# Kernel tuning notes

Hardware: AMD Instinct MI355X
Metric: run time of the kernel (lower is better)

Reference implementation:

```python
import jax, jax.numpy as jnp
import numpy as np

B = 1
T_DIM, H_DIM, W_DIM = 8, 24, 24          # video canvas (t, h, w)
TT, TH, TW = 2, 8, 8                      # tile sizes
WT, WH, WW = 6, 16, 16                    # window sizes (tokens)
HIDDEN = 1024
HEADS = 16
DH = HIDDEN // HEADS
SEQ = T_DIM * H_DIM * W_DIM               # 4608
NT, NH, NW = T_DIM // TT, H_DIM // TH, W_DIM // TW   # tile grid (4,3,3)
N_TILES = NT * NH * NW                    # 36
TILE = TT * TH * TW                       # 128


def _gather_indices():
    # STA tile mask: kv tile allowed iff |clamp(q_tile, k//2, n-1-k//2) - kv_tile| <= k//2 per axis.
    # Due to the clamp, every query tile attends to exactly the same number of kv tiles,
    # so the block-sparse pattern is a dense gather of shape [N_TILES, K].
    def axis(n, kernel_tiles):
        half = kernel_tiles // 2
        c = np.clip(np.arange(n), half, n - 1 - half)
        return c[:, None] + np.arange(-half, half + 1)[None, :]  # [n, 2*half+1]
    ts = axis(NT, WT // TT)
    hs = axis(NH, WH // TH)
    ws = axis(NW, WW // TW)
    idx = (ts[:, None, None, :, None, None] * NH
           + hs[None, :, None, None, :, None]) * NW \
          + ws[None, None, :, None, None, :]
    return idx.reshape(N_TILES, -1).astype(np.int32)  # [N_TILES, K]


def setup_inputs() -> dict:
    key = jax.random.key(0)
    k1, k2, k3, k4, k5 = jax.random.split(key, 5)
    s = 0.02
    return {
        "hidden_states": jax.random.normal(k1, (B, SEQ, HIDDEN), jnp.float32),
        "q_w": jax.random.normal(k2, (HIDDEN, HIDDEN), jnp.float32) * s,
        "k_w": jax.random.normal(k3, (HIDDEN, HIDDEN), jnp.float32) * s,
        "v_w": jax.random.normal(k4, (HIDDEN, HIDDEN), jnp.float32) * s,
        "o_w": jax.random.normal(k5, (HIDDEN, HIDDEN), jnp.float32) * s,
    }


def _tileize(x):
    # [B, S, HEADS*DH] -> [B, HEADS, N_TILES, TILE, DH] in (t,h,w) tile-major order
    x = x.reshape(B, NT, TT, NH, TH, NW, TW, HEADS, DH)
    x = x.transpose(0, 7, 1, 3, 5, 2, 4, 6, 8)
    return x.reshape(B, HEADS, N_TILES, TILE, DH)


def _untileize(x):
    # [B, HEADS, N_TILES, TILE, DH] -> [B, S, HEADS*DH]
    x = x.reshape(B, HEADS, NT, NH, NW, TT, TH, TW, DH)
    x = x.transpose(0, 2, 5, 3, 6, 4, 7, 1, 8)
    return x.reshape(B, SEQ, HEADS * DH)


def reference(hidden_states, q_w, k_w, v_w, o_w):
    q = _tileize(hidden_states @ q_w.T)
    k = _tileize(hidden_states @ k_w.T)
    v = _tileize(hidden_states @ v_w.T)
    idx = jnp.asarray(_gather_indices())          # [N_TILES, K] (static)
    kk = k[:, :, idx]                              # [B, H, N_TILES, K, TILE, DH]
    vv = v[:, :, idx]
    K = idx.shape[1]
    kk = kk.reshape(B, HEADS, N_TILES, K * TILE, DH)
    vv = vv.reshape(B, HEADS, N_TILES, K * TILE, DH)
    scale = 1.0 / np.sqrt(DH).astype(np.float32)
    scores = jnp.einsum('bhnqd,bhnkd->bhnqk', q * scale, kk)  # [B,H,nT,TILE,K*TILE]
    attn = jax.nn.softmax(scores, axis=-1)
    out = jnp.einsum('bhnqk,bhnkd->bhnqd', attn, vv)
    return _untileize(out) @ o_w.T
```

## Files before the change

kernel.cpp:

```cpp
#include <hip/hip_runtime.h>
#include <math.h>

#define HID 1024
#define NHEADS 16
#define NTILES 36
#define HEADSZ (36*128*64)
#define LOG2E 1.4426950408889634f
#define PLSTRIDE 73728

typedef unsigned short u16;
typedef unsigned int u32;
typedef __attribute__((ext_vector_type(8))) u16 ushort8v;
typedef __attribute__((ext_vector_type(8))) __bf16 bf16x8;
typedef __attribute__((ext_vector_type(16))) float f32x16;
typedef __attribute__((ext_vector_type(4))) u32 u32x4;

__device__ __forceinline__ u32 cvt_pk_bf16(float lo, float hi) {
  u32 r;
  asm("v_cvt_pk_bf16_f32 %0, %1, %2" : "=v"(r) : "v"(lo), "v"(hi));
  return r;
}
__device__ __forceinline__ void permlane32_swap(u32 &a, u32 &b) {
  asm volatile("v_permlane32_swap_b32 %0, %1" : "+v"(a), "+v"(b));
}
__device__ __forceinline__ void gld_lds16(const void* g, void* l) {
  __builtin_amdgcn_global_load_lds((const __attribute__((address_space(1))) u32*)g,
                                   (__attribute__((address_space(3))) u32*)l, 16, 0, 0);
}
__device__ __forceinline__ f32x16 mfma32(bf16x8 a, bf16x8 b, f32x16 c) {
  return __builtin_amdgcn_mfma_f32_32x32x16_bf16(a, b, c, 0, 0, 0);
}
__device__ __forceinline__ u16 bf16r(float x) {
  u32 b = __builtin_bit_cast(u32, x);
  b += 0x7fff + ((b >> 16) & 1);
  return (u16)(b >> 16);
}
__device__ __forceinline__ float bf2f(u16 v) {
  return __builtin_bit_cast(float, (u32)v << 16);
}

struct CastJob { const float* src[5]; u16* dst[5]; int n[5]; };

__global__ __launch_bounds__(256)
void cast_bf16(CastJob j) {
  const int w = blockIdx.y;
  const int n = j.n[w];
  const int i = (blockIdx.x * 256 + threadIdx.x) * 8;
  if (i >= n) return;
  const float4 v0 = *reinterpret_cast<const float4*>(j.src[w] + i);
  const float4 v1 = *reinterpret_cast<const float4*>(j.src[w] + i + 4);
  u32x4 o;
  o.x = cvt_pk_bf16(v0.x, v0.y);
  o.y = cvt_pk_bf16(v0.z, v0.w);
  o.z = cvt_pk_bf16(v1.x, v1.y);
  o.w = cvt_pk_bf16(v1.z, v1.w);
  *reinterpret_cast<u32x4*>(j.dst[w] + i) = o;
}

template<int AMODE, int CMODE, bool QKV, bool DBUF>
__global__ __launch_bounds__(256)
void gemm_mfma(const u16* __restrict__ A, const u16* __restrict__ B,
               void* __restrict__ Cv, float alpha)
{
    __shared__ __align__(16) u16 sm[DBUF ? 2 : 1][2][8192];

    const int tid = threadIdx.x;
    const int wv = tid >> 6, l = tid & 63;
    const int l31 = l & 31, hi = l >> 5;
    const int wm = wv >> 1, wn = wv & 1;
    const int by = blockIdx.y;
    const int n0 = blockIdx.x * 128;
    const float av = (QKV && n0 >= 1024) ? 1.0f : alpha;

    const int tt = by / 9, rem = by % 9, th = rem / 3, tw = rem % 3;
    const int tilebase = tt * 1152 + th * 192 + tw * 8;

    const int lrow = l >> 3;
    const int lslot = l & 7;
    const int sg = (lslot ^ lrow) * 8;
    const u16* aptr[4];
    const u16* bptr[4];
#pragma unroll
    for (int i = 0; i < 4; ++i) {
        const int row = (wv * 4 + i) * 8 + lrow;
        if (AMODE == 0) {
            const int s = tilebase + (row >> 6) * 576 + ((row >> 3) & 7) * 24 + (row & 7);
            aptr[i] = A + (size_t)s * HID + sg;
        } else {
            aptr[i] = A + (size_t)(by * 128 + row) * 64 + sg;
        }
        bptr[i] = B + (size_t)(n0 + row) * HID + sg;
    }

    auto stage = [&](int buf, int kc) {
#pragma unroll
        for (int i = 0; i < 4; ++i) {
            const u16* ga = (AMODE == 0) ? (aptr[i] + kc)
                                         : (aptr[i] + (size_t)(kc >> 6) * HEADSZ);
            gld_lds16(ga, &sm[buf][0][(wv * 4 + i) * 512]);
            gld_lds16(bptr[i] + kc, &sm[buf][1][(wv * 4 + i) * 512]);
        }
    };

    f32x16 acc[2][2];
#pragma unroll
    for (int mb = 0; mb < 2; ++mb)
#pragma unroll
        for (int nb = 0; nb < 2; ++nb)
#pragma unroll
            for (int i = 0; i < 16; ++i) acc[mb][nb][i] = 0.f;

    auto compute = [&](int buf) {
        __builtin_amdgcn_s_setprio(1);
#pragma unroll
        for (int kk = 0; kk < 4; ++kk) {
            bf16x8 af[2], bfr[2];
#pragma unroll
            for (int mb = 0; mb < 2; ++mb) {
                const int row = wm * 64 + mb * 32 + l31;
                af[mb] = *reinterpret_cast<const bf16x8*>(
                    &sm[buf][0][row * 64 + (((kk * 2 + hi) ^ (row & 7)) * 8)]);
            }
#pragma unroll
            for (int nb = 0; nb < 2; ++nb) {
                const int row = wn * 64 + nb * 32 + l31;
                bfr[nb] = *reinterpret_cast<const bf16x8*>(
                    &sm[buf][1][row * 64 + (((kk * 2 + hi) ^ (row & 7)) * 8)]);
            }
#pragma unroll
            for (int mb = 0; mb < 2; ++mb)
#pragma unroll
                for (int nb = 0; nb < 2; ++nb)
                    acc[mb][nb] = mfma32(af[mb], bfr[nb], acc[mb][nb]);
        }
        __builtin_amdgcn_s_setprio(0);
    };

    if (DBUF) {
        stage(0, 0);
        __syncthreads();
        int cur = 0;
        for (int kc = 0; kc < HID; kc += 64) {
            if (kc + 64 < HID) stage(cur ^ 1, kc + 64);
            compute(cur);
            __syncthreads();
            cur ^= 1;
        }
    } else {
        for (int kc = 0; kc < HID; kc += 64) {
            __syncthreads();
            stage(0, kc);
            __syncthreads();
            compute(0);
        }
    }

    if (CMODE == 0) {
        float* C = (float*)Cv;
#pragma unroll
        for (int mb = 0; mb < 2; ++mb)
#pragma unroll
            for (int r = 0; r < 16; ++r) {
                const int m = wm * 64 + mb * 32 + (r & 3) + 8 * (r >> 2) + 4 * hi;
                const int s = tilebase + (m >> 6) * 576 + ((m >> 3) & 7) * 24 + (m & 7);
#pragma unroll
                for (int nb = 0; nb < 2; ++nb) {
                    const int n = n0 + wn * 64 + nb * 32 + l31;
                    C[(size_t)s * HID + n] = acc[mb][nb][r] * av;
                }
            }
    } else {
        u16* C = (u16*)Cv;
#pragma unroll
        for (int mb = 0; mb < 2; ++mb)
#pragma unroll
            for (int rq = 0; rq < 4; ++rq) {
                const int mbase = wm * 64 + mb * 32 + 8 * rq + 4 * hi;
#pragma unroll
                for (int nb = 0; nb < 2; ++nb) {
                    const int n = n0 + wn * 64 + nb * 32 + l31;
                    const int head = n >> 6, dh = n & 63;
                    if (QKV && head >= 32) {
                        u32 w0 = cvt_pk_bf16(acc[mb][nb][rq * 4 + 0], acc[mb][nb][rq * 4 + 1]);
                        u32 w1 = cvt_pk_bf16(acc[mb][nb][rq * 4 + 2], acc[mb][nb][rq * 4 + 3]);
                        *reinterpret_cast<uint2*>(C + (size_t)head * HEADSZ +
                            (size_t)by * 8192 + dh * 128 + mbase) = make_uint2(w0, w1);
                    } else {
#pragma unroll
                        for (int j = 0; j < 4; ++j) {
                            const int m = mbase + j;
                            C[(size_t)head * HEADSZ + (size_t)(by * 128 + m) * 64 + dh] =
                                bf16r(acc[mb][nb][rq * 4 + j] * av);
                        }
                    }
                }
            }
    }
}

__global__ __launch_bounds__(256, 4)
void attn_mfma(const u16* __restrict__ Q, const u16* __restrict__ K,
               const u16* __restrict__ Vt, u16* __restrict__ pO0,
               u16* __restrict__ pO1, float* __restrict__ pl)
{
    __shared__ u16 sm[2][2][4096];

    const int tid = threadIdx.x;
    const int wave = tid >> 6;
    const int lane = tid & 63;
    const int l31 = lane & 31;
    const int hi  = lane >> 5;

    const int logical = (blockIdx.x & 7) * 144 + (blockIdx.x >> 3);
    const int p  = logical & 1;
    const int bt = logical >> 1;
    const int tl = bt % NTILES;
    const int hd = bt / NTILES;
    const size_t headbase = (size_t)hd * HEADSZ;

    const u16* Qg = Q + headbase + (size_t)tl * 8192;
    const u16* Kh = K + headbase;
    const u16* Vh = Vt + headbase;

    bf16x8 qf[4];
    {
        const u16* qrow = Qg + (wave * 32 + l31) * 64 + hi * 8;
#pragma unroll
        for (int ks = 0; ks < 4; ++ks)
            qf[ks] = *reinterpret_cast<const bf16x8*>(qrow + ks * 16);
    }

    const int base_t = (min(max(tl / 9, 1), 2) - 1) * 9;

    const int srow = lane >> 3;
    const int slot = lane & 7;

    auto stage = [&](int i, int bi) {
        const int kt = base_t + i;
        const u16* Kg = Kh + (size_t)kt * 8192 + p * 4096;
        const u16* Vg = Vh + (size_t)kt * 8192 + p * 64;
        u16* dk = &sm[bi][0][0];
        u16* dv = &sm[bi][1][0];
#pragma unroll
        for (int q = 0; q < 2; ++q) {
            const int seg = wave * 2 + q;
            const int key = seg * 8 + srow;
            gld_lds16(Kg + key * 64 + ((slot ^ (key & 7)) * 8), dk + seg * 512);
            const int dh = seg * 8 + srow;
            gld_lds16(Vg + dh * 128 + ((slot ^ (dh & 7)) * 8), dv + seg * 512);
        }
    };

    f32x16 accO0, accO1;
#pragma unroll
    for (int i = 0; i < 16; ++i) { accO0[i] = 0.f; accO1[i] = 0.f; }
    float lsum = 0.f;

    stage(0, 0);
    __syncthreads();

    for (int i = 0; i < 27; ++i) {
        const int cur = i & 1;
        if (i + 1 < 27) stage(i + 1, cur ^ 1);
        const u16* Ksb = &sm[cur][0][0];
        const u16* Vsb = &sm[cur][1][0];

#pragma unroll
        for (int c = 0; c < 2; ++c) {
            f32x16 s;
#pragma unroll
            for (int i2 = 0; i2 < 16; ++i2) s[i2] = 0.f;
            const int kr = c * 32 + l31;
            __builtin_amdgcn_s_setprio(1);
#pragma unroll
            for (int ks = 0; ks < 4; ++ks) {
                bf16x8 a = *reinterpret_cast<const bf16x8*>(
                    Ksb + kr * 64 + (((2 * ks + hi) ^ (kr & 7)) * 8));
                s = mfma32(a, qf[ks], s);
            }
            __builtin_amdgcn_s_setprio(0);

#pragma unroll
            for (int i2 = 0; i2 < 16; ++i2) s[i2] = __builtin_amdgcn_exp2f(s[i2]);

            float ps = 0.f;
#pragma unroll
            for (int i2 = 0; i2 < 16; ++i2) ps += s[i2];
            lsum += ps;

            bf16x8 pb[2];
            {
                u32 a0 = cvt_pk_bf16(s[0], s[1]);
                u32 a1 = cvt_pk_bf16(s[2], s[3]);
                u32 b0 = cvt_pk_bf16(s[4], s[5]);
                u32 b1 = cvt_pk_bf16(s[6], s[7]);
                permlane32_swap(a0, b0);
                permlane32_swap(a1, b1);
                u32x4 w; w.x = a0; w.y = a1; w.z = b0; w.w = b1;
                pb[0] = __builtin_bit_cast(bf16x8, w);
                u32 c0 = cvt_pk_bf16(s[8], s[9]);
                u32 c1 = cvt_pk_bf16(s[10], s[11]);
                u32 d0 = cvt_pk_bf16(s[12], s[13]);
                u32 d1 = cvt_pk_bf16(s[14], s[15]);
                permlane32_swap(c0, d0);
                permlane32_swap(c1, d1);
                u32x4 w2; w2.x = c0; w2.y = c1; w2.z = d0; w2.w = d1;
                pb[1] = __builtin_bit_cast(bf16x8, w2);
            }

            __builtin_amdgcn_s_setprio(1);
#pragma unroll
            for (int k2 = 0; k2 < 2; ++k2) {
                const int sg2 = c * 4 + k2 * 2 + hi;
                bf16x8 v0 = *reinterpret_cast<const bf16x8*>(
                    Vsb + l31 * 64 + ((sg2 ^ (l31 & 7)) * 8));
                accO0 = mfma32(v0, pb[k2], accO0);
                bf16x8 v1 = *reinterpret_cast<const bf16x8*>(
                    Vsb + (32 + l31) * 64 + ((sg2 ^ (l31 & 7)) * 8));
                accO1 = mfma32(v1, pb[k2], accO1);
            }
            __builtin_amdgcn_s_setprio(0);
        }
        __syncthreads();
    }

    lsum += __shfl_xor(lsum, 32);

    u16* Ob = (p ? pO1 : pO0) + ((size_t)bt * 128 + wave * 32 + l31) * 64;
#pragma unroll
    for (int t = 0; t < 4; ++t) {
        u32 p0 = cvt_pk_bf16(accO0[4 * t], accO0[4 * t + 1]);
        u32 p1 = cvt_pk_bf16(accO0[4 * t + 2], accO0[4 * t + 3]);
        *reinterpret_cast<uint2*>(Ob + t * 8 + 4 * hi) = make_uint2(p0, p1);
        u32 q0 = cvt_pk_bf16(accO1[4 * t], accO1[4 * t + 1]);
        u32 q1 = cvt_pk_bf16(accO1[4 * t + 2], accO1[4 * t + 3]);
        *reinterpret_cast<uint2*>(Ob + 32 + t * 8 + 4 * hi) = make_uint2(q0, q1);
    }
    if (hi == 0) pl[p * PLSTRIDE + bt * 128 + wave * 32 + l31] = lsum;
}

__global__ __launch_bounds__(256)
void merge_attn(const u16* __restrict__ pO0, const u16* __restrict__ pO1,
                const float* __restrict__ pl, u16* __restrict__ O)
{
    const int b = blockIdx.x;
    const int tid = threadIdx.x;
    const int row = tid >> 1;
    const int d0 = (tid & 1) * 32;
    const size_t rbase = ((size_t)b * 128 + row) * 64 + d0;
    const float inv = 1.f / (pl[b * 128 + row] + pl[PLSTRIDE + b * 128 + row]);
#pragma unroll
    for (int g = 0; g < 4; ++g) {
        ushort8v a = *reinterpret_cast<const ushort8v*>(pO0 + rbase + g * 8);
        ushort8v c = *reinterpret_cast<const ushort8v*>(pO1 + rbase + g * 8);
        u32 w[4];
#pragma unroll
        for (int h = 0; h < 4; ++h) {
            float f0 = (bf2f(a[2 * h])     + bf2f(c[2 * h]))     * inv;
            float f1 = (bf2f(a[2 * h + 1]) + bf2f(c[2 * h + 1])) * inv;
            w[h] = cvt_pk_bf16(f0, f1);
        }
        u32x4 st; st.x = w[0]; st.y = w[1]; st.z = w[2]; st.w = w[3];
        *reinterpret_cast<u32x4*>(O + rbase + g * 8) = st;
    }
}

extern "C" void kernel_launch(void* const* d_in, const int* in_sizes, int n_in,
                              void* d_out, int out_size, void* d_ws, size_t ws_size,
                              hipStream_t stream) {
    const float* hs = (const float*)d_in[0];
    const float* qw = (const float*)d_in[1];
    const float* kw = (const float*)d_in[2];
    const float* vw = (const float*)d_in[3];
    const float* ow = (const float*)d_in[4];
    float* out = (float*)d_out;

    const size_t TSZ = (size_t)NHEADS * HEADSZ;
    const size_t WSZ = (size_t)HID * HID;
    u16* hsb = (u16*)d_ws;
    u16* wqb = hsb + TSZ;
    u16* wkb = wqb + WSZ;
    u16* wvb = wkb + WSZ;
    u16* wob = wvb + WSZ;
    u16* qb  = wob + WSZ;
    u16* kb  = qb + TSZ;
    u16* vt  = kb + TSZ;
    u16* pO0 = hsb;
    u16* pO1 = vt + TSZ;
    float* pl = (float*)(pO1 + TSZ);
    u16* aob = (u16*)(pl + 2 * PLSTRIDE);

    CastJob cj;
    cj.src[0] = hs; cj.dst[0] = hsb; cj.n[0] = (int)TSZ;
    cj.src[1] = qw; cj.dst[1] = wqb; cj.n[1] = (int)WSZ;
    cj.src[2] = kw; cj.dst[2] = wkb; cj.n[2] = (int)WSZ;
    cj.src[3] = vw; cj.dst[3] = wvb; cj.n[3] = (int)WSZ;
    cj.src[4] = ow; cj.dst[4] = wob; cj.n[4] = (int)WSZ;
    cast_bf16<<<dim3(2304, 5), 256, 0, stream>>>(cj);

    gemm_mfma<0, 1, true, true><<<dim3(24, 36), 256, 0, stream>>>(hsb, wqb, qb, 0.125f * LOG2E);
    attn_mfma<<<NHEADS * NTILES * 2, 256, 0, stream>>>(qb, kb, vt, pO0, pO1, pl);
    merge_attn<<<NHEADS * NTILES, 256, 0, stream>>>(pO0, pO1, pl, aob);
    gemm_mfma<1, 0, false, true><<<dim3(8, 36), 256, 0, stream>>>(aob, wob, out, 1.0f);
}
```

Before: 158.7 us.

## Store V in MFMA-fragment layout and load it directly from global memory

The QKV projection epilogue now writes V transposed into a chunked layout: blocks of 8 keys, with 8 consecutive keys per head dimension stored contiguously. With that layout each lane's PV MFMA operand is one contiguous 16-byte global load. The attention kernel no longer stages V through LDS, which halves LDS traffic and footprint per stage. The cost is that V loads go to global/L2 memory inside the inner loop with no double buffering, so their latency may be exposed before the PV MFMAs.

After: 156.8 us (median of 2 runs). About the same (-1.2%).

```diff
diff --git a/kernel.cpp b/kernel.cpp
--- a/kernel.cpp
+++ b/kernel.cpp
@@ -184,7 +184,8 @@
                         u32 w0 = cvt_pk_bf16(acc[mb][nb][rq * 4 + 0], acc[mb][nb][rq * 4 + 1]);
                         u32 w1 = cvt_pk_bf16(acc[mb][nb][rq * 4 + 2], acc[mb][nb][rq * 4 + 3]);
                         *reinterpret_cast<uint2*>(C + (size_t)head * HEADSZ +
-                            (size_t)by * 8192 + dh * 128 + mbase) = make_uint2(w0, w1);
+                            (size_t)by * 8192 + (mbase >> 3) * 512 + (dh << 3) +
+                            (mbase & 7)) = make_uint2(w0, w1);
                     } else {
 #pragma unroll
                         for (int j = 0; j < 4; ++j) {
@@ -203,7 +204,7 @@
                const u16* __restrict__ Vt, u16* __restrict__ pO0,
                u16* __restrict__ pO1, float* __restrict__ pl)
 {
-    __shared__ u16 sm[2][2][4096];
+    __shared__ u16 sm[2][4096];
 
     const int tid = threadIdx.x;
     const int wave = tid >> 6;
@@ -238,16 +239,12 @@
     auto stage = [&](int i, int bi) {
         const int kt = base_t + i;
         const u16* Kg = Kh + (size_t)kt * 8192 + p * 4096;
-        const u16* Vg = Vh + (size_t)kt * 8192 + p * 64;
-        u16* dk = &sm[bi][0][0];
-        u16* dv = &sm[bi][1][0];
+        u16* dk = &sm[bi][0];
 #pragma unroll
         for (int q = 0; q < 2; ++q) {
             const int seg = wave * 2 + q;
             const int key = seg * 8 + srow;
             gld_lds16(Kg + key * 64 + ((slot ^ (key & 7)) * 8), dk + seg * 512);
-            const int dh = seg * 8 + srow;
-            gld_lds16(Vg + dh * 128 + ((slot ^ (dh & 7)) * 8), dv + seg * 512);
         }
     };
 
@@ -262,11 +259,20 @@
     for (int i = 0; i < 27; ++i) {
         const int cur = i & 1;
         if (i + 1 < 27) stage(i + 1, cur ^ 1);
-        const u16* Ksb = &sm[cur][0][0];
-        const u16* Vsb = &sm[cur][1][0];
+        const u16* Ksb = &sm[cur][0];
+        const u16* Vg = Vh + (size_t)(base_t + i) * 8192;
 
 #pragma unroll
         for (int c = 0; c < 2; ++c) {
+            bf16x8 vf[2][2];
+#pragma unroll
+            for (int k2 = 0; k2 < 2; ++k2) {
+                const int chunk = 8 * p + 4 * c + 2 * k2 + hi;
+                const u16* vb = Vg + chunk * 512 + l31 * 8;
+                vf[k2][0] = *reinterpret_cast<const bf16x8*>(vb);
+                vf[k2][1] = *reinterpret_cast<const bf16x8*>(vb + 256);
+            }
+
             f32x16 s;
 #pragma unroll
             for (int i2 = 0; i2 < 16; ++i2) s[i2] = 0.f;
@@ -311,13 +317,8 @@
             __builtin_amdgcn_s_setprio(1);
 #pragma unroll
             for (int k2 = 0; k2 < 2; ++k2) {
-                const int sg2 = c * 4 + k2 * 2 + hi;
-                bf16x8 v0 = *reinterpret_cast<const bf16x8*>(
-                    Vsb + l31 * 64 + ((sg2 ^ (l31 & 7)) * 8));
-                accO0 = mfma32(v0, pb[k2], accO0);
-                bf16x8 v1 = *reinterpret_cast<const bf16x8*>(
-                    Vsb + (32 + l31) * 64 + ((sg2 ^ (l31 & 7)) * 8));
-                accO1 = mfma32(v1, pb[k2], accO1);
+                accO0 = mfma32(vf[k2][0], pb[k2], accO0);
+                accO1 = mfma32(vf[k2][1], pb[k2], accO1);
             }
             __builtin_amdgcn_s_setprio(0);
         }
```
